# Optimization experiments

Measured on AMD Instinct MI355X. Metric: run time of the kernel, lower is better.

## Reference

```python
import jax, jax.numpy as jnp
import numpy as np

B, T, E, R, A, M = 64, 2000, 512, 1024, 512, 8


def setup_inputs() -> dict:
    key = jax.random.key(0)
    ks = jax.random.split(key, 9)
    attention_hidden_state = jax.random.normal(ks[0], (B, R), dtype=jnp.float32)
    memory = jax.random.normal(ks[1], (B, T, E), dtype=jnp.float32)
    previous_location = jax.random.uniform(ks[2], (B, 1, M), dtype=jnp.float32) * 10.0
    mask = jnp.zeros((B, T), dtype=bool)
    # F = Linear(R->A, bias, xavier tanh) -> Linear(A->A, no bias, xavier tanh) -> tanh -> lin(A->3M, bias)
    g = 5.0 / 3.0  # tanh gain
    lim1 = g * np.sqrt(6.0 / (R + A))
    W1 = jax.random.uniform(ks[3], (A, R), minval=-lim1, maxval=lim1, dtype=jnp.float32)
    b1 = jnp.zeros((A,), dtype=jnp.float32)
    lim2 = g * np.sqrt(6.0 / (A + A))
    W2 = jax.random.uniform(ks[4], (A, A), minval=-lim2, maxval=lim2, dtype=jnp.float32)
    lim3 = np.sqrt(1.0 / A)
    Wlin = jax.random.uniform(ks[5], (3 * M, A), minval=-lim3, maxval=lim3, dtype=jnp.float32) * 0.01
    blin = jax.random.uniform(ks[6], (3 * M,), minval=-lim3, maxval=lim3, dtype=jnp.float32) * 0.008 - 2.0
    return {"attention_hidden_state": attention_hidden_state, "memory": memory,
            "previous_location": previous_location, "mask": mask,
            "W1": W1, "b1": b1, "W2": W2, "Wlin": Wlin, "blin": blin}


def reference(attention_hidden_state, memory, previous_location, mask, W1, b1, W2, Wlin, blin):
    # normalize_attention_input=True
    h = jnp.tanh(attention_hidden_state)                       # (B, R)
    x = jnp.tanh((h @ W1.T + b1) @ W2.T)                       # (B, A) 2-layer variant
    y = (x @ Wlin.T + blin)[:, None, :]                        # (B, 1, 3M)
    m = y.shape[-1] // 3
    w, delta, scale = y[..., :m], y[..., m:2 * m], y[..., 2 * m:]
    delta = jax.nn.sigmoid(delta)                              # (B, 1, M)
    loc = previous_location + delta                            # (B, 1, M)
    scale = jax.nn.sigmoid(scale) * 2.0 + 1.0                  # (B, 1, M)
    pos = jnp.arange(memory.shape[1], dtype=memory.dtype)[None, :, None]  # (1, T, 1)
    d = loc - pos                                              # (B, T, M)
    z = 0.5 * (jax.lax.erf((d + 0.5) * scale) - jax.lax.erf((d - 0.5) * scale))
    wmix = jax.nn.sigmoid(w)[:, 0, :]                          # (B, M)
    alignment = jnp.einsum('btm,bm->bt', z, wmix)              # (B, T)
    alignment = jnp.where(mask, jnp.zeros((), alignment.dtype), alignment)  # score_mask_value=0
    attention_weights = jax.nn.softmax(alignment, axis=1)      # (B, T)
    attention_context = jnp.einsum('bt,bte->be', attention_weights, memory)  # (B, E)
    return attention_context, attention_weights, loc
```

## Files before the change

kernel.cpp:

```cpp
#include <hip/hip_runtime.h>
#include <math.h>

#define B 64
#define T 2000
#define E 512
#define R 1024
#define A 512
#define M 8

#define NCH 16
#define TCH (T / NCH)
#define NP  (NCH * 4)

typedef float nfloat4 __attribute__((ext_vector_type(4)));

__device__ __forceinline__ float sigmoidf_(float x) { return 1.0f / (1.0f + expf(-x)); }
__device__ __forceinline__ float dot4_(float4 a, float4 b) {
    return (a.x * b.x + a.y * b.y) + (a.z * b.z + a.w * b.w);
}

__global__ __launch_bounds__(512) void mlp_align_kernel(
    const float* __restrict__ ahs, const float* __restrict__ prev_loc,
    const unsigned char* __restrict__ mask,
    const float* __restrict__ W1, const float* __restrict__ b1,
    const float* __restrict__ W2, const float* __restrict__ Wlin,
    const float* __restrict__ blin,
    float* __restrict__ out_w,
    float* __restrict__ out_loc)
{
    __shared__ float sh_h[R];
    __shared__ float sh_t[A];
    __shared__ float sh_x[A];
    __shared__ float sh_y[3 * M];
    __shared__ float sh_wmix[M], sh_loc[M], sh_scale[M];
    __shared__ float sred[8];
    __shared__ float sbval;

    const int b = blockIdx.x;
    const int tid = threadIdx.x;
    const int wave = tid >> 6;
    const int lane = tid & 63;

    for (int k = tid; k < R; k += 512) sh_h[k] = tanhf(ahs[b * R + k]);
    __syncthreads();

    {
        const float4* h4 = (const float4*)sh_h;
        const float4 h0 = h4[lane], h1 = h4[lane + 64],
                     h2 = h4[lane + 128], h3 = h4[lane + 192];
        for (int j = 0; j < 64; j += 2) {
            const int ja = wave * 64 + j;
            const int jb = ja + 1;
            const float4* ra = (const float4*)(W1 + (size_t)ja * R);
            const float4* rb = (const float4*)(W1 + (size_t)jb * R);
            float4 a0 = ra[lane], a1 = ra[lane + 64], a2 = ra[lane + 128], a3 = ra[lane + 192];
            float4 c0 = rb[lane], c1 = rb[lane + 64], c2 = rb[lane + 128], c3 = rb[lane + 192];
            float accA = (dot4_(h0, a0) + dot4_(h1, a1)) + (dot4_(h2, a2) + dot4_(h3, a3));
            float accB = (dot4_(h0, c0) + dot4_(h1, c1)) + (dot4_(h2, c2) + dot4_(h3, c3));
#pragma unroll
            for (int off = 32; off > 0; off >>= 1) {
                accA += __shfl_down(accA, off);
                accB += __shfl_down(accB, off);
            }
            if (lane == 0) {
                sh_t[ja] = accA + b1[ja];
                sh_t[jb] = accB + b1[jb];
            }
        }
    }
    __syncthreads();

    {
        const float4* t4 = (const float4*)sh_t;
        const float4 t0 = t4[lane], t1 = t4[lane + 64];
        for (int j = 0; j < 64; j += 2) {
            const int ja = wave * 64 + j;
            const int jb = ja + 1;
            const float4* ra = (const float4*)(W2 + (size_t)ja * A);
            const float4* rb = (const float4*)(W2 + (size_t)jb * A);
            float4 a0 = ra[lane], a1 = ra[lane + 64];
            float4 c0 = rb[lane], c1 = rb[lane + 64];
            float accA = dot4_(t0, a0) + dot4_(t1, a1);
            float accB = dot4_(t0, c0) + dot4_(t1, c1);
#pragma unroll
            for (int off = 32; off > 0; off >>= 1) {
                accA += __shfl_down(accA, off);
                accB += __shfl_down(accB, off);
            }
            if (lane == 0) {
                sh_x[ja] = tanhf(accA);
                sh_x[jb] = tanhf(accB);
            }
        }
    }
    __syncthreads();

    if (tid < 16 * 3 * M) {
        const int i = tid >> 4;
        const int l16 = tid & 15;
        float s = 0.f;
        for (int k = l16; k < A; k += 16) s += sh_x[k] * Wlin[i * A + k];
        s += __shfl_down(s, 8, 16);
        s += __shfl_down(s, 4, 16);
        s += __shfl_down(s, 2, 16);
        s += __shfl_down(s, 1, 16);
        if (l16 == 0) sh_y[i] = s + blin[i];
    }
    __syncthreads();

    if (tid < M) {
        const int m = tid;
        const float delta = sigmoidf_(sh_y[M + m]);
        const float loc = prev_loc[b * M + m] + delta;
        sh_wmix[m]  = sigmoidf_(sh_y[m]);
        sh_loc[m]   = loc;
        sh_scale[m] = sigmoidf_(sh_y[2 * M + m]) * 2.0f + 1.0f;
        out_loc[b * M + m] = loc;
    }
    __syncthreads();

    float a[4];
    float lsum = 0.f;
#pragma unroll
    for (int i = 0; i < 4; ++i) {
        const int t = tid + i * 512;
        if (t < T) {
            const float tf = (float)t;
            float v = 0.f;
#pragma unroll
            for (int m = 0; m < M; ++m) {
                const float d = sh_loc[m] - tf;
                const float s = sh_scale[m];
                v += 0.5f * (erff((d + 0.5f) * s) - erff((d - 0.5f) * s)) * sh_wmix[m];
            }
            if (mask[b * T + t]) v = 0.f;
            a[i] = expf(v);
            lsum += a[i];
        } else {
            a[i] = 0.f;
        }
    }
#pragma unroll
    for (int off = 32; off > 0; off >>= 1) lsum += __shfl_down(lsum, off);
    if (lane == 0) sred[wave] = lsum;
    __syncthreads();
    if (tid == 0) {
        float s0 = 0.f;
        for (int i = 0; i < 8; ++i) s0 += sred[i];
        sbval = s0;
    }
    __syncthreads();
    const float inv = 1.0f / sbval;

#pragma unroll
    for (int i = 0; i < 4; ++i) {
        const int t = tid + i * 512;
        if (t < T) out_w[b * T + t] = a[i] * inv;
    }
}

__global__ __launch_bounds__(512) void context_partial_kernel(
    const float* __restrict__ memory,
    const float* __restrict__ w,
    float* __restrict__ partials)
{
    __shared__ float sh_w[TCH];

    const int b = blockIdx.x;
    const int chunk = blockIdx.y;
    const int tid = threadIdx.x;
    const int t0 = chunk * TCH;

    if (tid < TCH) sh_w[tid] = w[b * T + t0 + tid];
    __syncthreads();

    const int e4 = tid & 127;
    const int tp = tid >> 7;
    const nfloat4* mem4 = (const nfloat4*)(memory + (size_t)(b * T + t0) * E);

    float acc0 = 0.f, acc1 = 0.f, acc2 = 0.f, acc3 = 0.f;
#pragma unroll 4
    for (int t = tp; t < TCH; t += 4) {
        const float wv = sh_w[t];
        const nfloat4 mv = __builtin_nontemporal_load(&mem4[(size_t)t * (E / 4) + e4]);
        acc0 += wv * mv.x;
        acc1 += wv * mv.y;
        acc2 += wv * mv.z;
        acc3 += wv * mv.w;
    }

    nfloat4 accv = {acc0, acc1, acc2, acc3};
    nfloat4* dst = (nfloat4*)(partials + (((size_t)b * NCH + chunk) * 4 + tp) * E);
    dst[e4] = accv;
}

__global__ __launch_bounds__(256) void context_reduce_kernel(
    const float* __restrict__ partials,
    float* __restrict__ out_ctx)
{
    const int idx = blockIdx.x * 256 + threadIdx.x;
    const int b = idx >> 7;
    const int e4 = idx & 127;
    const float4* p = (const float4*)partials + (size_t)b * NP * (E / 4) + e4;
    float4 s = {0.f, 0.f, 0.f, 0.f};
#pragma unroll 8
    for (int c = 0; c < NP; ++c) {
        const float4 v = p[(size_t)c * (E / 4)];
        s.x += v.x; s.y += v.y; s.z += v.z; s.w += v.w;
    }
    ((float4*)out_ctx)[idx] = s;
}

extern "C" void kernel_launch(void* const* d_in, const int* in_sizes, int n_in,
                              void* d_out, int out_size, void* d_ws, size_t ws_size,
                              hipStream_t stream) {
    const float* ahs      = (const float*)d_in[0];
    const float* memory   = (const float*)d_in[1];
    const float* prev_loc = (const float*)d_in[2];
    const unsigned char* mask = (const unsigned char*)d_in[3];
    const float* W1   = (const float*)d_in[4];
    const float* b1   = (const float*)d_in[5];
    const float* W2   = (const float*)d_in[6];
    const float* Wlin = (const float*)d_in[7];
    const float* blin = (const float*)d_in[8];

    float* out = (float*)d_out;
    float* out_ctx = out;
    float* out_w   = out + B * E;
    float* out_loc = out + B * E + B * T;
    float* partials = (float*)d_ws;

    mlp_align_kernel<<<dim3(B), dim3(512), 0, stream>>>(
        ahs, prev_loc, mask, W1, b1, W2, Wlin, blin, out_w, out_loc);

    context_partial_kernel<<<dim3(B, NCH), dim3(512), 0, stream>>>(
        memory, out_w, partials);

    context_reduce_kernel<<<dim3((B * E / 4) / 256), dim3(256), 0, stream>>>(
        partials, out_ctx);
}
```

Measured before the change: 433.6 us.

## Move alignment and softmax into context kernel with deferred normalization

The erf-mixture alignment computation moves out of the per-batch MLP kernel, which now writes only the 24 mixture parameters per batch. Each (batch, chunk) block of the context kernel computes its own unnormalized exp weights and a partial sum. The finalize kernel divides both the context and the stored weights by the total. This spreads the erf work across 1024 blocks instead of 64 and removes the block-wide softmax reduction from the serial MLP kernel, at the cost of an extra read and write pass over the weights in finalize.

```diff
diff --git a/kernel.cpp b/kernel.cpp
--- a/kernel.cpp
+++ b/kernel.cpp
@@ -19,22 +19,18 @@
     return (a.x * b.x + a.y * b.y) + (a.z * b.z + a.w * b.w);
 }
 
-__global__ __launch_bounds__(512) void mlp_align_kernel(
+__global__ __launch_bounds__(512) void mlp_kernel(
     const float* __restrict__ ahs, const float* __restrict__ prev_loc,
-    const unsigned char* __restrict__ mask,
     const float* __restrict__ W1, const float* __restrict__ b1,
     const float* __restrict__ W2, const float* __restrict__ Wlin,
     const float* __restrict__ blin,
-    float* __restrict__ out_w,
+    float* __restrict__ params,
     float* __restrict__ out_loc)
 {
     __shared__ float sh_h[R];
     __shared__ float sh_t[A];
     __shared__ float sh_x[A];
     __shared__ float sh_y[3 * M];
-    __shared__ float sh_wmix[M], sh_loc[M], sh_scale[M];
-    __shared__ float sred[8];
-    __shared__ float sbval;
 
     const int b = blockIdx.x;
     const int tid = threadIdx.x;
@@ -112,67 +108,58 @@
         const int m = tid;
         const float delta = sigmoidf_(sh_y[M + m]);
         const float loc = prev_loc[b * M + m] + delta;
-        sh_wmix[m]  = sigmoidf_(sh_y[m]);
-        sh_loc[m]   = loc;
-        sh_scale[m] = sigmoidf_(sh_y[2 * M + m]) * 2.0f + 1.0f;
+        const float wmix = sigmoidf_(sh_y[m]);
+        const float scale = sigmoidf_(sh_y[2 * M + m]) * 2.0f + 1.0f;
         out_loc[b * M + m] = loc;
-    }
-    __syncthreads();
-
-    float a[4];
-    float lsum = 0.f;
-#pragma unroll
-    for (int i = 0; i < 4; ++i) {
-        const int t = tid + i * 512;
-        if (t < T) {
-            const float tf = (float)t;
-            float v = 0.f;
-#pragma unroll
-            for (int m = 0; m < M; ++m) {
-                const float d = sh_loc[m] - tf;
-                const float s = sh_scale[m];
-                v += 0.5f * (erff((d + 0.5f) * s) - erff((d - 0.5f) * s)) * sh_wmix[m];
-            }
-            if (mask[b * T + t]) v = 0.f;
-            a[i] = expf(v);
-            lsum += a[i];
-        } else {
-            a[i] = 0.f;
-        }
-    }
-#pragma unroll
-    for (int off = 32; off > 0; off >>= 1) lsum += __shfl_down(lsum, off);
-    if (lane == 0) sred[wave] = lsum;
-    __syncthreads();
-    if (tid == 0) {
-        float s0 = 0.f;
-        for (int i = 0; i < 8; ++i) s0 += sred[i];
-        sbval = s0;
-    }
-    __syncthreads();
-    const float inv = 1.0f / sbval;
-
-#pragma unroll
-    for (int i = 0; i < 4; ++i) {
-        const int t = tid + i * 512;
-        if (t < T) out_w[b * T + t] = a[i] * inv;
-    }
-}
-
-__global__ __launch_bounds__(512) void context_partial_kernel(
+        params[b * 24 + m]      = wmix;
+        params[b * 24 + 8 + m]  = loc;
+        params[b * 24 + 16 + m] = scale;
+    }
+}
+
+__global__ __launch_bounds__(512) void context_align_kernel(
     const float* __restrict__ memory,
-    const float* __restrict__ w,
-    float* __restrict__ partials)
+    const unsigned char* __restrict__ mask,
+    const float* __restrict__ params,
+    float* __restrict__ out_w,
+    float* __restrict__ partials,
+    float* __restrict__ psum)
 {
     __shared__ float sh_w[TCH];
+    __shared__ float sh_p[24];
 
     const int b = blockIdx.x;
     const int chunk = blockIdx.y;
     const int tid = threadIdx.x;
     const int t0 = chunk * TCH;
 
-    if (tid < TCH) sh_w[tid] = w[b * T + t0 + tid];
-    __syncthreads();
+    if (tid < 24) sh_p[tid] = params[b * 24 + tid];
+    __syncthreads();
+
+    if (tid < TCH) {
+        const int t = t0 + tid;
+        const float tf = (float)t;
+        float v = 0.f;
+#pragma unroll
+        for (int m = 0; m < M; ++m) {
+            const float d = sh_p[8 + m] - tf;
+            const float s = sh_p[16 + m];
+            v += 0.5f * (erff((d + 0.5f) * s) - erff((d - 0.5f) * s)) * sh_p[m];
+        }
+        if (mask[b * T + t]) v = 0.f;
+        const float e = expf(v);
+        sh_w[tid] = e;
+        out_w[b * T + t] = e;
+    }
+    __syncthreads();
+
+    if (tid < 64) {
+        float s = 0.f;
+        for (int k = tid; k < TCH; k += 64) s += sh_w[k];
+#pragma unroll
+        for (int off = 32; off > 0; off >>= 1) s += __shfl_down(s, off);
+        if (tid == 0) psum[b * NCH + chunk] = s;
+    }
 
     const int e4 = tid & 127;
     const int tp = tid >> 7;
@@ -194,21 +181,43 @@
     dst[e4] = accv;
 }
 
-__global__ __launch_bounds__(256) void context_reduce_kernel(
+__global__ __launch_bounds__(256) void finalize_kernel(
     const float* __restrict__ partials,
-    float* __restrict__ out_ctx)
+    const float* __restrict__ psum,
+    float* __restrict__ out_ctx,
+    float* __restrict__ out_w)
 {
-    const int idx = blockIdx.x * 256 + threadIdx.x;
-    const int b = idx >> 7;
-    const int e4 = idx & 127;
-    const float4* p = (const float4*)partials + (size_t)b * NP * (E / 4) + e4;
-    float4 s = {0.f, 0.f, 0.f, 0.f};
+    __shared__ float s_inv;
+    const int b = blockIdx.x;
+    const int tid = threadIdx.x;
+
+    if (tid < 64) {
+        float s = (tid < NCH) ? psum[b * NCH + tid] : 0.f;
+#pragma unroll
+        for (int off = 32; off > 0; off >>= 1) s += __shfl_down(s, off);
+        if (tid == 0) s_inv = 1.0f / s;
+    }
+    __syncthreads();
+    const float inv = s_inv;
+
+    if (tid < E / 4) {
+        const float4* p = (const float4*)partials + (size_t)b * NP * (E / 4) + tid;
+        float4 acc = {0.f, 0.f, 0.f, 0.f};
 #pragma unroll 8
-    for (int c = 0; c < NP; ++c) {
-        const float4 v = p[(size_t)c * (E / 4)];
-        s.x += v.x; s.y += v.y; s.z += v.z; s.w += v.w;
-    }
-    ((float4*)out_ctx)[idx] = s;
+        for (int c = 0; c < NP; ++c) {
+            const float4 v = p[(size_t)c * (E / 4)];
+            acc.x += v.x; acc.y += v.y; acc.z += v.z; acc.w += v.w;
+        }
+        float4 r = {acc.x * inv, acc.y * inv, acc.z * inv, acc.w * inv};
+        ((float4*)out_ctx)[b * (E / 4) + tid] = r;
+    }
+
+    float4* w4 = (float4*)(out_w + (size_t)b * T);
+    for (int i = tid; i < T / 4; i += 256) {
+        float4 v = w4[i];
+        v.x *= inv; v.y *= inv; v.z *= inv; v.w *= inv;
+        w4[i] = v;
+    }
 }
 
 extern "C" void kernel_launch(void* const* d_in, const int* in_sizes, int n_in,
@@ -228,14 +237,17 @@
     float* out_ctx = out;
     float* out_w   = out + B * E;
     float* out_loc = out + B * E + B * T;
+
     float* partials = (float*)d_ws;
-
-    mlp_align_kernel<<<dim3(B), dim3(512), 0, stream>>>(
-        ahs, prev_loc, mask, W1, b1, W2, Wlin, blin, out_w, out_loc);
-
-    context_partial_kernel<<<dim3(B, NCH), dim3(512), 0, stream>>>(
-        memory, out_w, partials);
-
-    context_reduce_kernel<<<dim3((B * E / 4) / 256), dim3(256), 0, stream>>>(
-        partials, out_ctx);
-}
+    float* psum     = partials + (size_t)B * NP * E;
+    float* params   = psum + B * NCH;
+
+    mlp_kernel<<<dim3(B), dim3(512), 0, stream>>>(
+        ahs, prev_loc, W1, b1, W2, Wlin, blin, params, out_loc);
+
+    context_align_kernel<<<dim3(B, NCH), dim3(512), 0, stream>>>(
+        memory, mask, params, out_w, partials, psum);
+
+    finalize_kernel<<<dim3(B), dim3(256), 0, stream>>>(
+        partials, psum, out_ctx, out_w);
+}
```

After: 429.7 us. No clear change (-0.9%).
